# Kernel optimization log

Hardware: AMD Instinct MI355X
Metric: run time of the kernel (lower is better)

The kernel has to match this reference:

```python
import jax, jax.numpy as jnp
import numpy as np

S, B, H, V = 64, 8, 512, 8192  # seq_length, batch, hidden, vocab
NEG = -1e9  # finite stand-in for -inf so gradients stay clean


def setup_inputs() -> dict:
    key = jax.random.key(0)
    ks = jax.random.split(key, 8)
    lin = lambda k, fi, fo: jax.random.normal(k, (fi, fo), jnp.float32) * 0.05
    return dict(
        h=jax.random.normal(ks[0], (S, B, H), jnp.float32) * 0.1,
        sentence=jax.random.randint(ks[1], (S, B), 0, V),
        t_W1=lin(ks[2], 2 * H, H), t_b1=jnp.zeros((H,), jnp.float32),
        t_W2=lin(ks[3], H, 1), t_b2=jnp.zeros((1,), jnp.float32),
        w_W1=lin(ks[4], 2 * H, H), w_b1=jnp.zeros((H,), jnp.float32),
        w_W2=lin(ks[5], H, V), w_b2=jnp.zeros((V,), jnp.float32),
    )


def _inside(h, sentence, t_W1, t_b1, t_W2, t_b2, w_W1, w_b1, w_W2, w_b2):
    sent_length = S - 1
    # ---- transition scores on full (i, j) grid: concat(h_i, h_j) -> MLP -> scalar
    hi = jnp.broadcast_to(h[:, None], (S, S, B, H))
    hj = jnp.broadcast_to(h[None, :], (S, S, B, H))
    feat = jnp.concatenate([hi, hj], axis=-1)                      # [S,S,B,2H]
    t = (jax.nn.relu(feat @ t_W1 + t_b1) @ t_W2 + t_b2)[..., 0]    # [S,S,B]
    sh_lp = jax.nn.log_sigmoid(-t)   # log p(shift | i, j)
    re_lp = jax.nn.log_sigmoid(t)    # log p(reduce | i, j)

    # ---- word generation log-probs for pairs (i, j), i < j <= sent_length-1
    iu, ju = jnp.triu_indices(sent_length, k=1)                    # P pairs
    hp = jnp.concatenate([h[iu], h[ju]], axis=-1)                  # [P,B,2H]
    logits = jax.nn.relu(hp @ w_W1 + w_b1) @ w_W2 + w_b2           # [P,B,V]
    lse = jax.scipy.special.logsumexp(logits, axis=-1)             # [P,B]
    tok = sentence[ju + 1]                                         # [P,B]
    tok_logit = jnp.take_along_axis(logits, tok[..., None], axis=-1)[..., 0]
    word_lp = tok_logit - lse
    # shift prob + word prob (word_prob_list in the original)
    wp = jnp.full((S, S, B), NEG, jnp.float32).at[iu, ju].set(sh_lp[iu, ju] + word_lp)

    # ---- DP table init
    table = jnp.full((S, S, B), NEG, jnp.float32)
    f0 = jnp.concatenate([h[0], h[0]], axis=-1)                    # [B,2H]
    lg0 = jax.nn.relu(f0 @ w_W1 + w_b1) @ w_W2 + w_b2              # [B,V]
    init_lp = jnp.take_along_axis(jax.nn.log_softmax(lg0, axis=-1),
                                  sentence[1][:, None], axis=1)[:, 0]
    table = table.at[0, 1].set(init_lp)
    jd = jnp.arange(1, sent_length)
    table = table.at[jd, jd + 1].set(0.0)

    # ---- diagonal sweep: table[i,j] = LSE_k( table[i,k]+table[k,j]+wp[i,k]+re[k,j] )
    ivec = jnp.arange(S)
    mvec = jnp.arange(1, S)

    def step(tab, g):
        i = ivec[:, None]
        m = mvec[None, :]
        k = jnp.clip(i + m, 0, S - 1)                              # [S,S-1]
        jv = jnp.clip(ivec + g, 0, S - 1)                          # [S]
        j = jv[:, None]
        valid = (m < g) & (ivec[:, None] + g <= sent_length)       # [S,S-1]
        sc = tab[i, k] + tab[k, j] + wp[i, k] + re_lp[k, j]        # [S,S-1,B]
        sc = jnp.where(valid[..., None], sc, NEG)
        mmax = jnp.max(sc, axis=1, keepdims=True)
        new = jnp.log(jnp.sum(jnp.exp(sc - mmax), axis=1)) + mmax[:, 0]
        row_ok = (ivec + g <= sent_length)[:, None]
        tab = tab.at[ivec, jv].set(jnp.where(row_ok, new, tab[ivec, jv]))
        return tab, None

    table, _ = jax.lax.scan(step, table, jnp.arange(2, sent_length + 1))
    final = table[0, sent_length] + re_lp[0, sent_length]          # [B]
    return -jnp.sum(final)  # neg_log_likelihood


def reference(h, sentence, t_W1, t_b1, t_W2, t_b2, w_W1, w_b1, w_W2, w_b2):
    return _inside(h, sentence, t_W1, t_b1, t_W2, t_b2, w_W1, w_b1, w_W2, w_b2)
```

## Files before the change

kernel.cpp:

```cpp
#include <hip/hip_runtime.h>
#include <hip/hip_bf16.h>
#include <hip/hip_fp8.h>
#include <math.h>

#define NEG (-1.0e9f)

typedef __bf16 bf16_t;
typedef __bf16 bf16x4 __attribute__((ext_vector_type(4)));
typedef __bf16 bf16x8 __attribute__((ext_vector_type(8)));
typedef float f32x4 __attribute__((ext_vector_type(4)));
typedef long i64x2 __attribute__((ext_vector_type(2)));
typedef unsigned char u8;
typedef unsigned long long u64;

#define SS 64
#define BB 8
#define HH 512
#define VV 8192
#define NPAIR 1953
#define NPTOT 1954
#define MROWS (NPTOT*BB)
#define MPAD  16384

__device__ __forceinline__ float logsig(float x) {
  return fminf(x, 0.f) - __logf(1.f + __expf(-fabsf(x)));
}
__device__ __forceinline__ u8 f2q(float x) { __hip_fp8_e4m3 q(x); return q.__x; }
__device__ __forceinline__ float q2f(u8 b) { __hip_fp8_e4m3 q; q.__x = b; return (float)q; }
__device__ __forceinline__ int ksl(int c) { return 2 * (c & 3) + (c >> 2); }

__global__ __launch_bounds__(256) void k_prep(
    const float* __restrict__ h,   bf16_t* __restrict__ hbf,
    const float* __restrict__ tW1, bf16_t* __restrict__ tW1T,
    const float* __restrict__ wW1, bf16_t* __restrict__ wW1T,
    const float* __restrict__ wW2, u8* __restrict__ w2t8) {
  __shared__ float tile[32][33];
  int blk = blockIdx.x, tid = threadIdx.x;
  if (blk < 256) {
    int gi = blk * 256 + tid;
    float4 v = ((const float4*)h)[gi];
    bf16x4 o = {(bf16_t)v.x, (bf16_t)v.y, (bf16_t)v.z, (bf16_t)v.w};
    ((bf16x4*)hbf)[gi] = o;
    return;
  }
  if (blk < 1280) {
    const float* in; bf16_t* out; int R = 1024, C = 512, t;
    if (blk < 768) { in = tW1; out = tW1T; t = blk - 256; }
    else           { in = wW1; out = wW1T; t = blk - 768; }
    int xt = C / 32;
    int c0 = (t % xt) * 32, r0 = (t / xt) * 32;
    int tx = tid & 31, ty = tid >> 5;
    for (int i = ty; i < 32; i += 8)
      tile[i][tx] = in[(size_t)(r0 + i) * C + c0 + tx];
    __syncthreads();
    for (int i = ty; i < 32; i += 8)
      out[(size_t)(c0 + i) * R + r0 + tx] = (bf16_t)tile[tx][i];
    return;
  }
  int t = blk - 1280;
  int c0 = (t % 256) * 32, r0 = (t / 256) * 32;
  int tx = tid & 31, ty = tid >> 5;
  for (int i = ty; i < 32; i += 8)
    tile[i][tx] = wW2[(size_t)(r0 + i) * 8192 + c0 + tx];
  __syncthreads();
  for (int i = ty; i < 32; i += 8) {
    int k = r0 + tx;
    int pos = (k >> 6) * 64 + ksl((k >> 3) & 7) * 8 + (k & 7);
    w2t8[(size_t)(c0 + i) * 512 + pos] = f2q(tile[tx][i]);
  }
}

__global__ __launch_bounds__(256) void k_gemm4(
    const bf16_t* __restrict__ A,
    const bf16_t* __restrict__ tW1T, const bf16_t* __restrict__ wW1T,
    float* __restrict__ Ut, float* __restrict__ Vt,
    float* __restrict__ Uw, float* __restrict__ Vw)
{
  __shared__ __align__(16) bf16_t As[128 * 32];
  __shared__ __align__(16) bf16_t Bs[128 * 32];
  const int tid = threadIdx.x;
  const int lane = tid & 63;
  const int wave = tid >> 6;
  const int wr = wave >> 1, wc = wave & 1;
  const int sel = blockIdx.x >> 4, sub = blockIdx.x & 15;
  const bf16_t* BT = (sel < 2 ? tW1T : wW1T) + (sel & 1) * 512;
  float* Cout = (sel == 0) ? Ut : (sel == 1) ? Vt : (sel == 2) ? Uw : Vw;
  const int m0 = (sub & 3) * 128, n0 = (sub >> 2) * 128;
  const int lda = 512, ldb = 1024, ldc = 512;

  const int rowS = tid >> 2;
  const int kS = (tid & 3) * 8;
  const bf16_t* gA0 = A + (size_t)(m0 + rowS) * lda + kS;
  const bf16_t* gA1 = A + (size_t)(m0 + rowS + 64) * lda + kS;
  const bf16_t* gB0 = BT + (size_t)(n0 + rowS) * ldb + kS;
  const bf16_t* gB1 = BT + (size_t)(n0 + rowS + 64) * ldb + kS;

  f32x4 acc[4][4] = {};
  const int aoff = (wr * 64 + (lane & 15)) * 32 + (lane >> 4) * 8;
  const int boff = (wc * 64 + (lane & 15)) * 32 + (lane >> 4) * 8;

  for (int k0 = 0; k0 < 512; k0 += 32) {
    __builtin_amdgcn_global_load_lds((const __attribute__((address_space(1))) void*)(gA0 + k0),
        (__attribute__((address_space(3))) void*)(As + wave * 512), 16, 0, 0);
    __builtin_amdgcn_global_load_lds((const __attribute__((address_space(1))) void*)(gA1 + k0),
        (__attribute__((address_space(3))) void*)(As + 2048 + wave * 512), 16, 0, 0);
    __builtin_amdgcn_global_load_lds((const __attribute__((address_space(1))) void*)(gB0 + k0),
        (__attribute__((address_space(3))) void*)(Bs + wave * 512), 16, 0, 0);
    __builtin_amdgcn_global_load_lds((const __attribute__((address_space(1))) void*)(gB1 + k0),
        (__attribute__((address_space(3))) void*)(Bs + 2048 + wave * 512), 16, 0, 0);
    __syncthreads();
    bf16x8 af[4], bfr[4];
    #pragma unroll
    for (int mf = 0; mf < 4; ++mf) af[mf] = *(const bf16x8*)&As[aoff + mf * 16 * 32];
    #pragma unroll
    for (int nf = 0; nf < 4; ++nf) bfr[nf] = *(const bf16x8*)&Bs[boff + nf * 16 * 32];
    #pragma unroll
    for (int mf = 0; mf < 4; ++mf)
      #pragma unroll
      for (int nf = 0; nf < 4; ++nf)
        acc[mf][nf] = __builtin_amdgcn_mfma_f32_16x16x32_bf16(af[mf], bfr[nf], acc[mf][nf], 0, 0, 0);
    __syncthreads();
  }
  #pragma unroll
  for (int mf = 0; mf < 4; ++mf)
    #pragma unroll
    for (int r2 = 0; r2 < 4; ++r2) {
      int grow = m0 + wr * 64 + mf * 16 + (lane >> 4) * 4 + r2;
      #pragma unroll
      for (int nf = 0; nf < 4; ++nf) {
        int gcol = n0 + wc * 64 + nf * 16 + (lane & 15);
        Cout[(size_t)grow * ldc + gcol] = acc[mf][nf][r2];
      }
    }
}

#define STAGEA(b, h, kt) do { \
  const u8* _s = A8 + (size_t)(m0 + (h)*128 + (tid>>2)) * 512 + (kt)*64 + csrc; \
  __builtin_amdgcn_global_load_lds((const __attribute__((address_space(1))) void*)_s, \
    (__attribute__((address_space(3))) void*)(As + (b)*16384 + (h)*8192 + (tid>>6)*1024), 16, 0, 0); \
} while(0)

#define STAGEB(b, h, kt) do { \
  const u8* _s = BT8 + (size_t)(n0 + (h)*128 + (tid>>2)) * 512 + (kt)*64 + csrc; \
  __builtin_amdgcn_global_load_lds((const __attribute__((address_space(1))) void*)_s, \
    (__attribute__((address_space(3))) void*)(Bs + (b)*16384 + (h)*8192 + (tid>>6)*1024), 16, 0, 0); \
} while(0)

#define LDA(b, mh) do { \
  _Pragma("unroll") \
  for (int _m = 0; _m < 4; ++_m) \
    afv[_m] = *(const i64x2*)(As + (b)*16384 + (mh)*8192 + ardE + _m*1024); \
} while(0)

#define LDB(b, nh) do { \
  _Pragma("unroll") \
  for (int _n = 0; _n < 2; ++_n) \
    bfv[nh][_n] = *(const i64x2*)(Bs + (b)*16384 + (nh)*8192 + brdE + _n*1024); \
} while(0)

#define MMA(mh, nh) do { \
  __builtin_amdgcn_s_setprio(1); \
  _Pragma("unroll") \
  for (int _m = 0; _m < 4; ++_m) \
    _Pragma("unroll") \
    for (int _n = 0; _n < 2; ++_n) { \
      acc[(mh)*4+_m][(nh)*2+_n] = __builtin_amdgcn_mfma_f32_16x16x32_fp8_fp8( \
          afv[_m][0], bfv[nh][_n][0], acc[(mh)*4+_m][(nh)*2+_n], 0, 0, 0); \
      acc[(mh)*4+_m][(nh)*2+_n] = __builtin_amdgcn_mfma_f32_16x16x32_fp8_fp8( \
          afv[_m][1], bfv[nh][_n][1], acc[(mh)*4+_m][(nh)*2+_n], 0, 0, 0); \
    } \
  __builtin_amdgcn_s_setprio(0); \
} while(0)

#define BARLG() do { __builtin_amdgcn_s_barrier(); \
  asm volatile("s_waitcnt lgkmcnt(0)" ::: "memory"); \
  __builtin_amdgcn_sched_barrier(0); } while(0)
#define ENDPH() __builtin_amdgcn_s_barrier()
#define CKPT() asm volatile("s_waitcnt vmcnt(2)" ::: "memory")

__global__ __launch_bounds__(512, 2) void k_gemm256(
    const u8* __restrict__ A8,
    const u8* __restrict__ BT8,
    const float* __restrict__ bias,
    float* __restrict__ sumexp)
{
  __shared__ __align__(16) u8 As[2 * 16384];
  __shared__ __align__(16) u8 Bs[2 * 16384];
  const int tid = threadIdx.x;
  const int l = tid & 63;
  const int wave = tid >> 6;
  const int wr = wave >> 2, wc = wave & 3;

  const int xcd = blockIdx.x & 7, sub = blockIdx.x >> 3;
  const int mt = xcd * 8 + (sub & 7);
  const int nt = sub >> 3;
  const int m0 = mt * 256, n0 = nt * 256;

  const int csrc = (((tid & 3) ^ ((tid >> 3) & 3)) << 4);
  const int rsw = (((l >> 4) ^ ((l & 15) >> 1)) & 3) << 4;
  const int ardE = (wr * 64 + (l & 15)) * 64 + rsw;
  const int brdE = (wc * 32 + (l & 15)) * 64 + rsw;

  f32x4 acc[8][4] = {};
  i64x2 afv[4];
  i64x2 bfv[2][2];

  STAGEA(0, 0, 0); STAGEA(0, 1, 0); STAGEB(0, 0, 0); STAGEB(0, 1, 0);
  STAGEA(1, 0, 1); STAGEB(1, 0, 1);
  CKPT();
  __builtin_amdgcn_s_barrier();

  #pragma unroll 1
  for (int t = 0; t < 4; ++t) {
    int tA = 2 * t + 1;
    int tB = 2 * t + 2; if (tB > 7) tB = 7;
    int tC = 2 * t + 3; if (tC > 7) tC = 7;
    LDA(0, 0); LDB(0, 0); STAGEA(1, 1, tA); BARLG(); MMA(0, 0); ENDPH();
    LDB(0, 1);            STAGEB(1, 1, tA); BARLG(); MMA(0, 1); ENDPH();
    LDA(0, 1);            STAGEA(0, 0, tB); BARLG(); MMA(1, 0); ENDPH();
                          STAGEB(0, 0, tB); BARLG(); MMA(1, 1); CKPT(); ENDPH();
    LDA(1, 0); LDB(1, 0); STAGEA(0, 1, tB); BARLG(); MMA(0, 0); ENDPH();
    LDB(1, 1);            STAGEB(0, 1, tB); BARLG(); MMA(0, 1); ENDPH();
    LDA(1, 1);            STAGEA(1, 0, tC); BARLG(); MMA(1, 0); ENDPH();
                          STAGEB(1, 0, tC); BARLG(); MMA(1, 1); CKPT(); ENDPH();
  }

  float b2v[4];
  #pragma unroll
  for (int nf = 0; nf < 4; ++nf)
    b2v[nf] = bias[n0 + (nf >> 1) * 128 + wc * 32 + (nf & 1) * 16 + (l & 15)];
  #pragma unroll
  for (int mf = 0; mf < 8; ++mf) {
    #pragma unroll
    for (int r2 = 0; r2 < 4; ++r2) {
      float s = 0.f;
      #pragma unroll
      for (int nf = 0; nf < 4; ++nf)
        s += __expf(acc[mf][nf][r2] + b2v[nf]);
      s += __shfl_xor(s, 1); s += __shfl_xor(s, 2);
      s += __shfl_xor(s, 4); s += __shfl_xor(s, 8);
      if ((l & 15) == 0)
        atomicAdd(&sumexp[m0 + (mf >> 2) * 128 + wr * 64 + (mf & 3) * 16 + (l >> 4) * 4 + r2], s);
    }
  }
}

__global__ __launch_bounds__(256) void k_act(const float* __restrict__ Uw, const float* __restrict__ Vw,
                                             const float* __restrict__ b1, u8* __restrict__ act8,
                                             float* __restrict__ sumexp) {
  int p = blockIdx.x;
  if (threadIdx.x < 8) sumexp[p * 8 + threadIdx.x] = 0.f;
  int iu = 0, ju = 0;
  bool real = (p < NPTOT);
  if (p < NPAIR) {
    int i = 0, base = 0;
    while (base + (62 - i) <= p) { base += 62 - i; ++i; }
    iu = i; ju = i + 1 + (p - base);
  }
  for (int t = threadIdx.x; t < 512; t += 256) {
    int b = t >> 6, c = t & 63;
    u64 bytes = 0;
    if (real) {
      const float4* u4 = (const float4*)(Uw + (size_t)(iu * BB + b) * HH);
      const float4* v4 = (const float4*)(Vw + (size_t)(ju * BB + b) * HH);
      const float4* bb4 = (const float4*)b1;
      #pragma unroll
      for (int q = 0; q < 2; ++q) {
        float4 uu = u4[c * 2 + q], vv = v4[c * 2 + q], bb = bb4[c * 2 + q];
        bytes |= (u64)f2q(fmaxf(uu.x + vv.x + bb.x, 0.f)) << (8 * (q * 4 + 0));
        bytes |= (u64)f2q(fmaxf(uu.y + vv.y + bb.y, 0.f)) << (8 * (q * 4 + 1));
        bytes |= (u64)f2q(fmaxf(uu.z + vv.z + bb.z, 0.f)) << (8 * (q * 4 + 2));
        bytes |= (u64)f2q(fmaxf(uu.w + vv.w + bb.w, 0.f)) << (8 * (q * 4 + 3));
      }
    }
    *(u64*)(act8 + (size_t)(p * 8 + b) * 512 + (c >> 3) * 64 + ksl(c & 7) * 8) = bytes;
  }
}

__global__ __launch_bounds__(256) void k_tnet(const float* __restrict__ Ut, const float* __restrict__ Vt,
                                              const float* __restrict__ b1, const float* __restrict__ W2,
                                              const float* __restrict__ b2,
                                              float* __restrict__ sh_lp, float* __restrict__ re_lp) {
  int gid = blockIdx.x * 4 + (threadIdx.x >> 6);
  int lane = threadIdx.x & 63;
  int b = gid & 7, j = (gid >> 3) & 63, i = gid >> 9;
  const float4* u = (const float4*)(Ut + (size_t)(i * BB + b) * HH);
  const float4* v = (const float4*)(Vt + (size_t)(j * BB + b) * HH);
  const float4* bb = (const float4*)b1;
  const float4* ww = (const float4*)W2;
  float s = 0.f;
  #pragma unroll
  for (int qq = 0; qq < 2; ++qq) {
    int c = lane * 2 + qq;
    float4 uu = u[c], vv = v[c], b4 = bb[c], w4 = ww[c];
    s += fmaxf(uu.x + vv.x + b4.x, 0.f) * w4.x;
    s += fmaxf(uu.y + vv.y + b4.y, 0.f) * w4.y;
    s += fmaxf(uu.z + vv.z + b4.z, 0.f) * w4.z;
    s += fmaxf(uu.w + vv.w + b4.w, 0.f) * w4.w;
  }
  #pragma unroll
  for (int off = 1; off < 64; off <<= 1) s += __shfl_xor(s, off);
  if (lane == 0) {
    float t = s + b2[0];
    re_lp[gid] = logsig(t);
    sh_lp[gid] = logsig(-t);
  }
}

__global__ __launch_bounds__(256) void k_toklogit(const u8* __restrict__ act8, const u8* __restrict__ w2t8,
                                                  const float* __restrict__ b2, const int* __restrict__ sent,
                                                  float* __restrict__ tok_logit) {
  int r = blockIdx.x * 4 + (threadIdx.x >> 6);
  int lane = threadIdx.x & 63;
  int p = r >> 3, b = r & 7;
  int tok;
  if (p >= NPAIR) {
    tok = sent[1 * BB + b];
  } else {
    int i = 0, base = 0;
    while (base + (62 - i) <= p) { base += 62 - i; ++i; }
    int ju = i + 1 + (p - base);
    tok = sent[(ju + 1) * BB + b];
  }
  u64 av = *(const u64*)(act8 + (size_t)r * 512 + lane * 8);
  u64 wv = *(const u64*)(w2t8 + (size_t)tok * 512 + lane * 8);
  float s = 0.f;
  #pragma unroll
  for (int e = 0; e < 8; ++e)
    s += q2f((u8)(av >> (8 * e))) * q2f((u8)(wv >> (8 * e)));
  #pragma unroll
  for (int off = 1; off < 64; off <<= 1) s += __shfl_xor(s, off);
  if (lane == 0) tok_logit[r] = s + b2[tok];
}

__global__ __launch_bounds__(1024) void k_dp(const float* __restrict__ sh_lp, const float* __restrict__ re_lp,
                                             const float* __restrict__ tok_logit, const float* __restrict__ sumexp,
                                             float* __restrict__ finals) {
  int b = blockIdx.x;
  __shared__ float tab[4096];
  __shared__ float wpl[4096];
  __shared__ float rel[4096];
  int tid = threadIdx.x;
  for (int idx = tid; idx < 4096; idx += 1024) {
    tab[idx] = NEG;
    int i = idx >> 6, j = idx & 63;
    float w = NEG;
    if (i < j && j <= 62) {
      int p = i * 62 - i * (i - 1) / 2 + (j - i - 1);
      int r = p * 8 + b;
      w = sh_lp[idx * 8 + b] + (tok_logit[r] - __logf(sumexp[r]));
    }
    wpl[idx] = w;
    rel[idx] = re_lp[idx * 8 + b];
  }
  __syncthreads();
  if (tid == 0) tab[1] = tok_logit[NPAIR * 8 + b] - __logf(sumexp[NPAIR * 8 + b]);
  if (tid >= 1 && tid <= 62) tab[tid * 64 + tid + 1] = 0.f;
  __syncthreads();
  int lane = tid & 63, wave = tid >> 6;
  for (int g = 2; g <= 63; ++g) {
    int cnt = 64 - g;
    if (g <= 17) {
      int seg = lane >> 4, sl = lane & 15;
      int i = wave * 4 + seg;
      if (i < cnt) {
        int m = sl + 1;
        int j = i + g, k = i + m;
        float sc = NEG;
        if (m < g) sc = tab[i * 64 + k] + tab[k * 64 + j] + wpl[i * 64 + k] + rel[k * 64 + j];
        float mx = sc;
        #pragma unroll
        for (int off = 1; off < 16; off <<= 1) mx = fmaxf(mx, __shfl_xor(mx, off));
        float e = (m < g) ? __expf(sc - mx) : 0.f;
        #pragma unroll
        for (int off = 1; off < 16; off <<= 1) e += __shfl_xor(e, off);
        if (sl == 0) tab[i * 64 + j] = __logf(e) + mx;
      }
    } else {
      for (int i = wave; i < cnt; i += 16) {
        int m = lane + 1;
        int j = i + g, k = i + m;
        float sc = NEG;
        if (m < g) sc = tab[i * 64 + k] + tab[k * 64 + j] + wpl[i * 64 + k] + rel[k * 64 + j];
        float mx = sc;
        #pragma unroll
        for (int off = 1; off < 64; off <<= 1) mx = fmaxf(mx, __shfl_xor(mx, off));
        float e = (m < g) ? __expf(sc - mx) : 0.f;
        #pragma unroll
        for (int off = 1; off < 64; off <<= 1) e += __shfl_xor(e, off);
        if (lane == 0) tab[i * 64 + j] = __logf(e) + mx;
      }
    }
    __syncthreads();
  }
  if (tid == 0) finals[b] = tab[63] + rel[63];
}

__global__ void k_final(const float* __restrict__ finals, float* __restrict__ out) {
  if (threadIdx.x == 0) {
    float s = 0.f;
    for (int b = 0; b < 8; ++b) s += finals[b];
    out[0] = -s;
  }
}

extern "C" void kernel_launch(void* const* d_in, const int* in_sizes, int n_in,
                              void* d_out, int out_size, void* d_ws, size_t ws_size,
                              hipStream_t stream) {
  const float* h    = (const float*)d_in[0];
  const int*   sent = (const int*)d_in[1];
  const float* tW1  = (const float*)d_in[2];
  const float* tb1  = (const float*)d_in[3];
  const float* tW2  = (const float*)d_in[4];
  const float* tb2  = (const float*)d_in[5];
  const float* wW1  = (const float*)d_in[6];
  const float* wb1  = (const float*)d_in[7];
  const float* wW2  = (const float*)d_in[8];
  const float* wb2  = (const float*)d_in[9];
  float* out = (float*)d_out;

  char* ws = (char*)d_ws;
  size_t off = 0;
  auto alloc = [&](size_t bytes) { char* p = ws + off; off += (bytes + 255) & ~(size_t)255; return p; };
  bf16_t* hbf    = (bf16_t*)alloc((size_t)512 * 512 * 2);
  bf16_t* tW1T   = (bf16_t*)alloc((size_t)512 * 1024 * 2);
  bf16_t* wW1T   = (bf16_t*)alloc((size_t)512 * 1024 * 2);
  u8*     w2t8   = (u8*)alloc((size_t)VV * HH);
  float*  Ut     = (float*)alloc((size_t)512 * 512 * 4);
  float*  Vt     = (float*)alloc((size_t)512 * 512 * 4);
  float*  Uw     = (float*)alloc((size_t)512 * 512 * 4);
  float*  Vw     = (float*)alloc((size_t)512 * 512 * 4);
  u8*     act8   = (u8*)alloc((size_t)MPAD * HH);
  float*  sumexp = (float*)alloc((size_t)MPAD * 4);
  float*  tokl   = (float*)alloc((size_t)MPAD * 4);
  float*  shlp   = (float*)alloc((size_t)32768 * 4);
  float*  relp   = (float*)alloc((size_t)32768 * 4);
  float*  finals = (float*)alloc(256);

  k_prep<<<5376, 256, 0, stream>>>(h, hbf, tW1, tW1T, wW1, wW1T, wW2, w2t8);
  k_gemm4<<<64, 256, 0, stream>>>(hbf, tW1T, wW1T, Ut, Vt, Uw, Vw);
  k_act<<<MPAD / 8, 256, 0, stream>>>(Uw, Vw, wb1, act8, sumexp);
  k_tnet<<<32768 / 4, 256, 0, stream>>>(Ut, Vt, tb1, tW2, tb2, shlp, relp);
  k_gemm256<<<2048, 512, 0, stream>>>(act8, w2t8, wb2, sumexp);
  k_toklogit<<<MROWS / 4, 256, 0, stream>>>(act8, w2t8, wb2, sent, tokl);
  k_dp<<<8, 1024, 0, stream>>>(shlp, relp, tokl, sumexp, finals);
  k_final<<<1, 64, 0, stream>>>(finals, out);
}
```

Measured before the change: 297.5 us.

## Use 32x32x64 scaled FP8 MFMA in vocab GEMM and fuse token-logit into k_act

Switches the large vocab logsumexp GEMM from 16x16x32 fp8 MFMA to the gfx950 32x32x64 f8f6f4 scaled MFMA with unit scales. This changes the LDS read addressing, the operand and accumulator layout, the load schedule and the epilogue reduction, and drops the K-slot permutation from the act8 and w2t8 layouts. The target-token logit dot product now runs inside k_act from data already in registers, which removes the separate k_toklogit launch and its reread of act8. The cost is that B fragments are reloaded each phase, and the epilogue needs wider shuffle reductions.

After: 322.4 us. +8.4%, slower.

```diff
diff --git a/kernel.cpp b/kernel.cpp
--- a/kernel.cpp
+++ b/kernel.cpp
@@ -9,7 +9,9 @@
 typedef __bf16 bf16x4 __attribute__((ext_vector_type(4)));
 typedef __bf16 bf16x8 __attribute__((ext_vector_type(8)));
 typedef float f32x4 __attribute__((ext_vector_type(4)));
-typedef long i64x2 __attribute__((ext_vector_type(2)));
+typedef float f32x16 __attribute__((ext_vector_type(16)));
+typedef int i32x4 __attribute__((ext_vector_type(4)));
+typedef int i32x8 __attribute__((ext_vector_type(8)));
 typedef unsigned char u8;
 typedef unsigned long long u64;
 
@@ -27,7 +29,6 @@
 }
 __device__ __forceinline__ u8 f2q(float x) { __hip_fp8_e4m3 q(x); return q.__x; }
 __device__ __forceinline__ float q2f(u8 b) { __hip_fp8_e4m3 q; q.__x = b; return (float)q; }
-__device__ __forceinline__ int ksl(int c) { return 2 * (c & 3) + (c >> 2); }
 
 __global__ __launch_bounds__(256) void k_prep(
     const float* __restrict__ h,   bf16_t* __restrict__ hbf,
@@ -63,11 +64,8 @@
   for (int i = ty; i < 32; i += 8)
     tile[i][tx] = wW2[(size_t)(r0 + i) * 8192 + c0 + tx];
   __syncthreads();
-  for (int i = ty; i < 32; i += 8) {
-    int k = r0 + tx;
-    int pos = (k >> 6) * 64 + ksl((k >> 3) & 7) * 8 + (k & 7);
-    w2t8[(size_t)(c0 + i) * 512 + pos] = f2q(tile[tx][i]);
-  }
+  for (int i = ty; i < 32; i += 8)
+    w2t8[(size_t)(c0 + i) * 512 + r0 + tx] = f2q(tile[tx][i]);
 }
 
 __global__ __launch_bounds__(256) void k_gemm4(
@@ -147,28 +145,28 @@
 } while(0)
 
 #define LDA(b, mh) do { \
-  _Pragma("unroll") \
-  for (int _m = 0; _m < 4; ++_m) \
-    afv[_m] = *(const i64x2*)(As + (b)*16384 + (mh)*8192 + ardE + _m*1024); \
+  i32x4 _l0 = *(const i32x4*)(As + (b)*16384 + (mh)*8192 + aoff0); \
+  i32x4 _h0 = *(const i32x4*)(As + (b)*16384 + (mh)*8192 + aoff1); \
+  aF0 = __builtin_shufflevector(_l0, _h0, 0,1,2,3,4,5,6,7); \
+  i32x4 _l1 = *(const i32x4*)(As + (b)*16384 + (mh)*8192 + aoff0 + 2048); \
+  i32x4 _h1 = *(const i32x4*)(As + (b)*16384 + (mh)*8192 + aoff1 + 2048); \
+  aF1 = __builtin_shufflevector(_l1, _h1, 0,1,2,3,4,5,6,7); \
 } while(0)
 
 #define LDB(b, nh) do { \
-  _Pragma("unroll") \
-  for (int _n = 0; _n < 2; ++_n) \
-    bfv[nh][_n] = *(const i64x2*)(Bs + (b)*16384 + (nh)*8192 + brdE + _n*1024); \
+  i32x4 _l = *(const i32x4*)(Bs + (b)*16384 + (nh)*8192 + boff0); \
+  i32x4 _h = *(const i32x4*)(Bs + (b)*16384 + (nh)*8192 + boff1); \
+  bF = __builtin_shufflevector(_l, _h, 0,1,2,3,4,5,6,7); \
 } while(0)
+
+#define ACC(mh, ms, nh) acc[(mh)*4 + (ms)*2 + (nh)]
 
 #define MMA(mh, nh) do { \
   __builtin_amdgcn_s_setprio(1); \
-  _Pragma("unroll") \
-  for (int _m = 0; _m < 4; ++_m) \
-    _Pragma("unroll") \
-    for (int _n = 0; _n < 2; ++_n) { \
-      acc[(mh)*4+_m][(nh)*2+_n] = __builtin_amdgcn_mfma_f32_16x16x32_fp8_fp8( \
-          afv[_m][0], bfv[nh][_n][0], acc[(mh)*4+_m][(nh)*2+_n], 0, 0, 0); \
-      acc[(mh)*4+_m][(nh)*2+_n] = __builtin_amdgcn_mfma_f32_16x16x32_fp8_fp8( \
-          afv[_m][1], bfv[nh][_n][1], acc[(mh)*4+_m][(nh)*2+_n], 0, 0, 0); \
-    } \
+  ACC(mh,0,nh) = __builtin_amdgcn_mfma_scale_f32_32x32x64_f8f6f4( \
+      aF0, bF, ACC(mh,0,nh), 0, 0, 0, 0x7F7F7F7F, 0, 0x7F7F7F7F); \
+  ACC(mh,1,nh) = __builtin_amdgcn_mfma_scale_f32_32x32x64_f8f6f4( \
+      aF1, bF, ACC(mh,1,nh), 0, 0, 0, 0x7F7F7F7F, 0, 0x7F7F7F7F); \
   __builtin_amdgcn_s_setprio(0); \
 } while(0)
 
@@ -197,13 +195,18 @@
   const int m0 = mt * 256, n0 = nt * 256;
 
   const int csrc = (((tid & 3) ^ ((tid >> 3) & 3)) << 4);
-  const int rsw = (((l >> 4) ^ ((l & 15) >> 1)) & 3) << 4;
-  const int ardE = (wr * 64 + (l & 15)) * 64 + rsw;
-  const int brdE = (wc * 32 + (l & 15)) * 64 + rsw;
-
-  f32x4 acc[8][4] = {};
-  i64x2 afv[4];
-  i64x2 bfv[2][2];
+  const int u0 = (l >> 5) * 2;
+  const int rA = wr * 64 + (l & 31);
+  const int sA = (rA >> 1) & 3;
+  const int aoff0 = rA * 64 + ((u0 ^ sA) << 4);
+  const int aoff1 = rA * 64 + (((u0 + 1) ^ sA) << 4);
+  const int rB = wc * 32 + (l & 31);
+  const int sB = (rB >> 1) & 3;
+  const int boff0 = rB * 64 + ((u0 ^ sB) << 4);
+  const int boff1 = rB * 64 + (((u0 + 1) ^ sB) << 4);
+
+  f32x16 acc[8] = {};
+  i32x8 aF0, aF1, bF;
 
   STAGEA(0, 0, 0); STAGEA(0, 1, 0); STAGEB(0, 0, 0); STAGEB(0, 1, 0);
   STAGEA(1, 0, 1); STAGEB(1, 0, 1);
@@ -217,37 +220,41 @@
     int tC = 2 * t + 3; if (tC > 7) tC = 7;
     LDA(0, 0); LDB(0, 0); STAGEA(1, 1, tA); BARLG(); MMA(0, 0); ENDPH();
     LDB(0, 1);            STAGEB(1, 1, tA); BARLG(); MMA(0, 1); ENDPH();
-    LDA(0, 1);            STAGEA(0, 0, tB); BARLG(); MMA(1, 0); ENDPH();
-                          STAGEB(0, 0, tB); BARLG(); MMA(1, 1); CKPT(); ENDPH();
+    LDA(0, 1); LDB(0, 0); STAGEA(0, 0, tB); BARLG(); MMA(1, 0); ENDPH();
+    LDB(0, 1);            STAGEB(0, 0, tB); BARLG(); MMA(1, 1); CKPT(); ENDPH();
     LDA(1, 0); LDB(1, 0); STAGEA(0, 1, tB); BARLG(); MMA(0, 0); ENDPH();
     LDB(1, 1);            STAGEB(0, 1, tB); BARLG(); MMA(0, 1); ENDPH();
-    LDA(1, 1);            STAGEA(1, 0, tC); BARLG(); MMA(1, 0); ENDPH();
-                          STAGEB(1, 0, tC); BARLG(); MMA(1, 1); CKPT(); ENDPH();
-  }
-
-  float b2v[4];
+    LDA(1, 1); LDB(1, 0); STAGEA(1, 0, tC); BARLG(); MMA(1, 0); ENDPH();
+    LDB(1, 1);            STAGEB(1, 0, tC); BARLG(); MMA(1, 1); CKPT(); ENDPH();
+  }
+
+  float b2v0 = bias[n0 + wc * 32 + (l & 31)];
+  float b2v1 = bias[n0 + 128 + wc * 32 + (l & 31)];
+  const int hf = (l >> 5) * 4;
   #pragma unroll
-  for (int nf = 0; nf < 4; ++nf)
-    b2v[nf] = bias[n0 + (nf >> 1) * 128 + wc * 32 + (nf & 1) * 16 + (l & 15)];
-  #pragma unroll
-  for (int mf = 0; mf < 8; ++mf) {
-    #pragma unroll
-    for (int r2 = 0; r2 < 4; ++r2) {
-      float s = 0.f;
-      #pragma unroll
-      for (int nf = 0; nf < 4; ++nf)
-        s += __expf(acc[mf][nf][r2] + b2v[nf]);
-      s += __shfl_xor(s, 1); s += __shfl_xor(s, 2);
-      s += __shfl_xor(s, 4); s += __shfl_xor(s, 8);
-      if ((l & 15) == 0)
-        atomicAdd(&sumexp[m0 + (mf >> 2) * 128 + wr * 64 + (mf & 3) * 16 + (l >> 4) * 4 + r2], s);
+  for (int mh = 0; mh < 2; ++mh) {
+    #pragma unroll
+    for (int ms = 0; ms < 2; ++ms) {
+      f32x16 A0 = ACC(mh, ms, 0), A1 = ACC(mh, ms, 1);
+      #pragma unroll
+      for (int rg = 0; rg < 16; ++rg) {
+        float s = __expf(A0[rg] + b2v0) + __expf(A1[rg] + b2v1);
+        s += __shfl_xor(s, 1); s += __shfl_xor(s, 2);
+        s += __shfl_xor(s, 4); s += __shfl_xor(s, 8);
+        s += __shfl_xor(s, 16);
+        if ((l & 31) == 0)
+          atomicAdd(&sumexp[m0 + mh * 128 + wr * 64 + ms * 32 + (rg & 3) + 8 * (rg >> 2) + hf], s);
+      }
     }
   }
 }
 
 __global__ __launch_bounds__(256) void k_act(const float* __restrict__ Uw, const float* __restrict__ Vw,
                                              const float* __restrict__ b1, u8* __restrict__ act8,
-                                             float* __restrict__ sumexp) {
+                                             float* __restrict__ sumexp,
+                                             const u8* __restrict__ w2t8, const int* __restrict__ sent,
+                                             const float* __restrict__ b2, float* __restrict__ tok_logit) {
+  __shared__ float pd[512];
   int p = blockIdx.x;
   if (threadIdx.x < 8) sumexp[p * 8 + threadIdx.x] = 0.f;
   int iu = 0, ju = 0;
@@ -257,6 +264,7 @@
     while (base + (62 - i) <= p) { base += 62 - i; ++i; }
     iu = i; ju = i + 1 + (p - base);
   }
+  const int srow = (p < NPAIR) ? (ju + 1) : 1;
   for (int t = threadIdx.x; t < 512; t += 256) {
     int b = t >> 6, c = t & 63;
     u64 bytes = 0;
@@ -273,7 +281,31 @@
         bytes |= (u64)f2q(fmaxf(uu.w + vv.w + bb.w, 0.f)) << (8 * (q * 4 + 3));
       }
     }
-    *(u64*)(act8 + (size_t)(p * 8 + b) * 512 + (c >> 3) * 64 + ksl(c & 7) * 8) = bytes;
+    *(u64*)(act8 + (size_t)(p * 8 + b) * 512 + c * 8) = bytes;
+    float s = 0.f;
+    if (real) {
+      int tok = sent[srow * BB + b];
+      u64 wv = *(const u64*)(w2t8 + (size_t)tok * 512 + c * 8);
+      #pragma unroll
+      for (int e = 0; e < 8; ++e)
+        s += q2f((u8)(bytes >> (8 * e))) * q2f((u8)(wv >> (8 * e)));
+    }
+    pd[t] = s;
+  }
+  __syncthreads();
+  if (real) {
+    int wv_ = threadIdx.x >> 6, ln = threadIdx.x & 63;
+    #pragma unroll
+    for (int rr = 0; rr < 2; ++rr) {
+      int b = wv_ * 2 + rr;
+      float s = pd[b * 64 + ln];
+      #pragma unroll
+      for (int off = 1; off < 64; off <<= 1) s += __shfl_xor(s, off);
+      if (ln == 0) {
+        int tok = sent[srow * BB + b];
+        tok_logit[p * 8 + b] = s + b2[tok];
+      }
+    }
   }
 }
 
@@ -305,32 +337,6 @@
     re_lp[gid] = logsig(t);
     sh_lp[gid] = logsig(-t);
   }
-}
-
-__global__ __launch_bounds__(256) void k_toklogit(const u8* __restrict__ act8, const u8* __restrict__ w2t8,
-                                                  const float* __restrict__ b2, const int* __restrict__ sent,
-                                                  float* __restrict__ tok_logit) {
-  int r = blockIdx.x * 4 + (threadIdx.x >> 6);
-  int lane = threadIdx.x & 63;
-  int p = r >> 3, b = r & 7;
-  int tok;
-  if (p >= NPAIR) {
-    tok = sent[1 * BB + b];
-  } else {
-    int i = 0, base = 0;
-    while (base + (62 - i) <= p) { base += 62 - i; ++i; }
-    int ju = i + 1 + (p - base);
-    tok = sent[(ju + 1) * BB + b];
-  }
-  u64 av = *(const u64*)(act8 + (size_t)r * 512 + lane * 8);
-  u64 wv = *(const u64*)(w2t8 + (size_t)tok * 512 + lane * 8);
-  float s = 0.f;
-  #pragma unroll
-  for (int e = 0; e < 8; ++e)
-    s += q2f((u8)(av >> (8 * e))) * q2f((u8)(wv >> (8 * e)));
-  #pragma unroll
-  for (int off = 1; off < 64; off <<= 1) s += __shfl_xor(s, off);
-  if (lane == 0) tok_logit[r] = s + b2[tok];
 }
 
 __global__ __launch_bounds__(1024) void k_dp(const float* __restrict__ sh_lp, const float* __restrict__ re_lp,
@@ -439,10 +445,9 @@
 
   k_prep<<<5376, 256, 0, stream>>>(h, hbf, tW1, tW1T, wW1, wW1T, wW2, w2t8);
   k_gemm4<<<64, 256, 0, stream>>>(hbf, tW1T, wW1T, Ut, Vt, Uw, Vw);
-  k_act<<<MPAD / 8, 256, 0, stream>>>(Uw, Vw, wb1, act8, sumexp);
+  k_act<<<MPAD / 8, 256, 0, stream>>>(Uw, Vw, wb1, act8, sumexp, w2t8, sent, wb2, tokl);
   k_tnet<<<32768 / 4, 256, 0, stream>>>(Ut, Vt, tb1, tW2, tb2, shlp, relp);
   k_gemm256<<<2048, 512, 0, stream>>>(act8, w2t8, wb2, sumexp);
-  k_toklogit<<<MROWS / 4, 256, 0, stream>>>(act8, w2t8, wb2, sent, tokl);
   k_dp<<<8, 1024, 0, stream>>>(shlp, relp, tokl, sumexp, finals);
   k_final<<<1, 64, 0, stream>>>(finals, out);
 }
```
